# Kernel tuning notes

Hardware: AMD Instinct MI355X
Metric: run time of the kernel (lower is better)

The kernel has to match this reference:

```python
import jax, jax.numpy as jnp
import numpy as np

B = 8192
FL = 96      # feature_len
K = 3        # dynamic filter kernel size
NOUT = 2
EPS = 1e-5
P = (K - 1) // 2

def _lrelu(x):
    return jnp.where(x >= 0, x, 0.1 * x)

def _conv1d(x, w, b):
    # x: [b,1,L], w: [1,1,3], b: [1]; padding=1, stride=1
    y = jax.lax.conv_general_dilated(x, w, (1,), [(1, 1)], dimension_numbers=('NCH', 'OIH', 'NCH'))
    return y + b[None, :, None]

def _bn(y, g, be, m, v):
    # eval-mode BatchNorm1d with running stats
    return (y - m) / jnp.sqrt(v + EPS) * g + be


def setup_inputs() -> dict:
    key = jax.random.key(0)
    ks = jax.random.split(key, 40)
    d = {'x': jax.random.normal(ks[0], (B, 576), jnp.float32)}
    # trans_layer: 6 conv1d (1->1, k=3)
    for i in range(6):
        d[f'cw{i+1}'] = jax.random.normal(ks[1 + i], (1, 1, 3), jnp.float32) * 0.4
        d[f'cb{i+1}'] = jax.random.normal(ks[7 + i], (1,), jnp.float32) * 0.1
    # fusion_layer.de_dimen: Linear(FL -> K*K)
    d['de_W'] = jax.random.normal(ks[13], (K * K, FL), jnp.float32) * 0.1
    d['de_b'] = jnp.zeros((K * K,), jnp.float32)
    # reshape_layer: Linear(2*FL -> 3*FL) + BN
    d['rs_W'] = jax.random.normal(ks[14], (3 * FL, 2 * FL), jnp.float32) * 0.07
    d['rs_b'] = jnp.zeros((3 * FL,), jnp.float32)
    d['rs_g'] = 1.0 + 0.1 * jax.random.normal(ks[15], (3 * FL,), jnp.float32)
    d['rs_be'] = 0.1 * jax.random.normal(ks[16], (3 * FL,), jnp.float32)
    d['rs_m'] = 0.05 * jax.random.normal(ks[17], (3 * FL,), jnp.float32)
    d['rs_v'] = jax.random.uniform(ks[18], (3 * FL,), jnp.float32, 0.5, 1.5)
    # classifier_shallow: Linear(6*FL -> 3*FL) + BN + ReLU + Linear(3*FL -> NOUT)
    d['cl_W1'] = jax.random.normal(ks[19], (3 * FL, 6 * FL), jnp.float32) * 0.05
    d['cl_b1'] = jnp.zeros((3 * FL,), jnp.float32)
    d['cl_g'] = 1.0 + 0.1 * jax.random.normal(ks[20], (3 * FL,), jnp.float32)
    d['cl_be'] = 0.1 * jax.random.normal(ks[21], (3 * FL,), jnp.float32)
    d['cl_m'] = 0.05 * jax.random.normal(ks[22], (3 * FL,), jnp.float32)
    d['cl_v'] = jax.random.uniform(ks[23], (3 * FL,), jnp.float32, 0.5, 1.5)
    d['cl_W2'] = jax.random.normal(ks[24], (NOUT, 3 * FL), jnp.float32) * 0.05
    d['cl_b2'] = jnp.zeros((NOUT,), jnp.float32)
    return d


def reference(x, cw1, cb1, cw2, cb2, cw3, cb3, cw4, cb4, cw5, cb5, cw6, cb6,
              de_W, de_b, rs_W, rs_b, rs_g, rs_be, rs_m, rs_v,
              cl_W1, cl_b1, cl_g, cl_be, cl_m, cl_v, cl_W2, cl_b2):
    def trans(c):  # c: [b,1,3*FL] -> three [b,1,FL]
        s1, s2, s3 = c[..., :FL], c[..., FL:2 * FL], c[..., 2 * FL:]
        x1 = _lrelu(_conv1d(s1, cw1, cb1))
        x2 = _lrelu(_conv1d(s2, cw2, cb2))
        x3 = _lrelu(_conv1d(s3, cw3, cb3))
        return (_lrelu(_conv1d(x1, cw4, cb4)),
                _lrelu(_conv1d(x2, cw5, cb5)),
                _lrelu(_conv1d(x3, cw6, cb6)))

    def fusion(arm, x86, bert):  # each [b,1,FL]
        b = arm.shape[0]
        # c==1 so matmul(s_1^T, s_2) is a per-sample outer product: [b,FL,FL]
        m = _lrelu(jnp.einsum('bl,bm->blm', arm[:, 0], x86[:, 0]))
        # per-sample 3x3 dynamic filter from bert embedding
        s3 = _lrelu(bert[:, 0] @ de_W.T + de_b).reshape(b, 1, K, K)
        fe = jax.lax.conv_general_dilated(
            m.reshape(1, b, FL, FL), s3, (1, 1), [(P, P), (P, P)],
            feature_group_count=b, dimension_numbers=('NCHW', 'OIHW', 'NCHW'))
        fe = _lrelu(fe).reshape(b, FL, FL)
        # AvgPool1d(FL) == mean over last dim (and over rows for the permuted map)
        return jnp.concatenate([fe.mean(axis=2), fe.mean(axis=1)], axis=1)  # [b,2*FL]

    def resh(e):
        return _lrelu(_bn(e @ rs_W.T + rs_b, rs_g, rs_be, rs_m, rs_v))

    xu = x[:, None, :]  # unsqueeze(dim=1)
    c1, c2 = xu[..., :3 * FL], xu[..., 3 * FL:]
    e1 = resh(fusion(*trans(c1))) + c1[:, 0]
    e2 = resh(fusion(*trans(c2))) + c2[:, 0]
    ce = jnp.concatenate([e1, e2], axis=1)  # [b,6*FL]
    # Dropout is identity in eval mode
    h = jax.nn.relu(_bn(ce @ cl_W1.T + cl_b1, cl_g, cl_be, cl_m, cl_v))
    return h @ cl_W2.T + cl_b2  # [b,NOUT]
```

## Files before the change

kernel.cpp:

```cpp
#include <hip/hip_runtime.h>
#include <hip/hip_bf16.h>
#include <math.h>

#define FLn 96
#define SEG 288
#define EPRE_DIM 192
#define EPS_BN 1e-5f

typedef __attribute__((ext_vector_type(8))) short short8;
typedef __attribute__((ext_vector_type(4))) float floatx4;

__device__ __forceinline__ float lrelu(float v) { return fmaxf(v, 0.1f * v); }
__device__ __forceinline__ short f2bf(float f) {
  __hip_bfloat16 h = __float2bfloat16(f);
  return *reinterpret_cast<short*>(&h);
}

__global__ __launch_bounds__(256) void k0_cast(
    const float* __restrict__ rsW, const float* __restrict__ clW1,
    __hip_bfloat16* __restrict__ wB2, __hip_bfloat16* __restrict__ wB3) {
  int idx = blockIdx.x * 256 + threadIdx.x;
  int stride = gridDim.x * 256;
  for (int i = idx; i < 288 * 192; i += stride) wB2[i] = __float2bfloat16(rsW[i]);
  for (int i = idx; i < 288 * 576; i += stride) wB3[i] = __float2bfloat16(clW1[i]);
}

#define O_CIN 0
#define O_ST1 288
#define O_APP 576
#define O_ANP 674
#define O_XPP 772
#define O_XNP 870
#define O_BERT 968
#define O_WKER 1064
#define O_ABF 1088
#define O_BBF 1472
#define O_RP 0
#define SLICE 2048

__global__ __launch_bounds__(256) void k1_persample(
    const float* __restrict__ x,
    const float* __restrict__ cw1, const float* __restrict__ cb1,
    const float* __restrict__ cw2, const float* __restrict__ cb2,
    const float* __restrict__ cw3, const float* __restrict__ cb3,
    const float* __restrict__ cw4, const float* __restrict__ cb4,
    const float* __restrict__ cw5, const float* __restrict__ cb5,
    const float* __restrict__ cw6, const float* __restrict__ cb6,
    const float* __restrict__ deW, const float* __restrict__ deb,
    __hip_bfloat16* __restrict__ epre) {
  __shared__ float sl[4 * SLICE];
  const int tid = threadIdx.x;
  const int wave = tid >> 6;
  const int lane = tid & 63;
  const int quad = lane >> 4;
  const int l16 = lane & 15;
  const int unit = blockIdx.x * 4 + wave;
  float* S = sl + wave * SLICE;
  short* Ssh = (short*)S;
  const float* xrow = x + (size_t)(unit >> 1) * 576 + (unit & 1) * 288;

  const float a0w0 = cw1[0], a0w1 = cw1[1], a0w2 = cw1[2], a0b = cb1[0];
  const float a1w0 = cw2[0], a1w1 = cw2[1], a1w2 = cw2[2], a1b = cb2[0];
  const float a2w0 = cw3[0], a2w1 = cw3[1], a2w2 = cw3[2], a2b = cb3[0];
  const float b0w0 = cw4[0], b0w1 = cw4[1], b0w2 = cw4[2], b0b = cb4[0];
  const float b1w0 = cw5[0], b1w1 = cw5[1], b1w2 = cw5[2], b1b = cb5[0];
  const float b2w0 = cw6[0], b2w1 = cw6[1], b2w2 = cw6[2], b2b = cb6[0];

  for (int t4 = lane; t4 < 72; t4 += 64)
    *(float4*)&S[O_CIN + 4 * t4] = ((const float4*)xrow)[t4];
  if (lane < 8) S[576 + 98 * (lane >> 1) + (lane & 1) * 97] = 0.f;

  for (int t = lane; t < SEG; t += 64) {
    bool g1 = t >= 96, g2 = t >= 192;
    float wa = g2 ? a2w0 : (g1 ? a1w0 : a0w0);
    float wb = g2 ? a2w1 : (g1 ? a1w1 : a0w1);
    float wc = g2 ? a2w2 : (g1 ? a1w2 : a0w2);
    float bb = g2 ? a2b  : (g1 ? a1b  : a0b);
    int p = t - (g2 ? 192 : (g1 ? 96 : 0));
    float l = p > 0 ? S[O_CIN + t - 1] : 0.f;
    float m = S[O_CIN + t];
    float r = p < FLn - 1 ? S[O_CIN + t + 1] : 0.f;
    S[O_ST1 + t] = lrelu(fmaf(wa, l, fmaf(wb, m, fmaf(wc, r, bb))));
  }
  for (int t = lane; t < SEG; t += 64) {
    bool g1 = t >= 96, g2 = t >= 192;
    float wa = g2 ? b2w0 : (g1 ? b1w0 : b0w0);
    float wb = g2 ? b2w1 : (g1 ? b1w1 : b0w1);
    float wc = g2 ? b2w2 : (g1 ? b1w2 : b0w2);
    float bb = g2 ? b2b  : (g1 ? b1b  : b0b);
    int p = t - (g2 ? 192 : (g1 ? 96 : 0));
    float l = p > 0 ? S[O_ST1 + t - 1] : 0.f;
    float m = S[O_ST1 + t];
    float r = p < FLn - 1 ? S[O_ST1 + t + 1] : 0.f;
    float v = lrelu(fmaf(wa, l, fmaf(wb, m, fmaf(wc, r, bb))));
    if (!g1) {
      S[O_APP + 1 + p] = fmaxf(v, 0.1f * v);
      S[O_ANP + 1 + p] = fminf(v, 0.1f * v);
    } else if (!g2) {
      S[O_XPP + 1 + p] = fmaxf(v, 0.f);
      S[O_XNP + 1 + p] = fminf(v, 0.f);
    } else {
      S[O_BERT + p] = v;
    }
  }
  if (quad < 3) {
    float bv[6];
#pragma unroll
    for (int k = 0; k < 6; ++k) bv[k] = S[O_BERT + l16 + 16 * k];
#pragma unroll
    for (int oi = 0; oi < 3; ++oi) {
      int o = quad * 3 + oi;
      float p = 0.f;
#pragma unroll
      for (int k = 0; k < 6; ++k) p = fmaf(bv[k], deW[o * 96 + l16 + 16 * k], p);
      p += __shfl_xor(p, 1, 16);
      p += __shfl_xor(p, 2, 16);
      p += __shfl_xor(p, 4, 16);
      p += __shfl_xor(p, 8, 16);
      if (l16 == 0) S[O_WKER + o] = lrelu(p + deb[o]);
    }
  }
  float w9[9];
#pragma unroll
  for (int q = 0; q < 9; ++q) w9[q] = S[O_WKER + q];

  for (int t = lane; t < 96; t += 64) {
    float xp0 = S[O_XPP + t], xp1 = S[O_XPP + t + 1], xp2 = S[O_XPP + t + 2];
    float xn0 = S[O_XNP + t], xn1 = S[O_XNP + t + 1], xn2 = S[O_XNP + t + 2];
    short8 b;
#pragma unroll
    for (int d = 0; d < 3; ++d) {
      float cp = fmaf(w9[3 * d], xp0, fmaf(w9[3 * d + 1], xp1, w9[3 * d + 2] * xp2));
      float cn = fmaf(w9[3 * d], xn0, fmaf(w9[3 * d + 1], xn1, w9[3 * d + 2] * xn2));
      b[d] = f2bf(cp);
      b[3 + d] = f2bf(cn);
    }
    b[6] = 0; b[7] = 0;
    *(short8*)&Ssh[2 * O_BBF + t * 8] = b;
  }
  for (int m = lane; m < 96; m += 64) {
    short8 a;
    a[0] = f2bf(S[O_APP + m]);
    a[1] = f2bf(S[O_APP + m + 1]);
    a[2] = f2bf(S[O_APP + m + 2]);
    a[3] = f2bf(S[O_ANP + m]);
    a[4] = f2bf(S[O_ANP + m + 1]);
    a[5] = f2bf(S[O_ANP + m + 2]);
    a[6] = 0; a[7] = 0;
    *(short8*)&Ssh[2 * O_ABF + m * 8] = a;
  }

  short8 aF[6];
#pragma unroll
  for (int mt = 0; mt < 6; ++mt) {
    short8 t = *(const short8*)&Ssh[2 * O_ABF + (mt * 16 + l16) * 8];
#pragma unroll
    for (int j = 0; j < 8; ++j) aF[mt][j] = (quad == 0) ? t[j] : (short)0;
  }

  float rowpart[6][4];
#pragma unroll
  for (int mt = 0; mt < 6; ++mt)
#pragma unroll
    for (int r = 0; r < 4; ++r) rowpart[mt][r] = 0.f;
  float cs[6];
#pragma unroll
  for (int s = 0; s < 6; ++s) cs[s] = 0.f;

#pragma unroll
  for (int s = 0; s < 6; ++s) {
    short8 tb = *(const short8*)&Ssh[2 * O_BBF + (s * 16 + l16) * 8];
    short8 bF;
#pragma unroll
    for (int j = 0; j < 8; ++j) bF[j] = (quad == 0) ? tb[j] : (short)0;
    floatx4 accv[6];
#pragma unroll
    for (int mt = 0; mt < 6; ++mt)
      accv[mt] = __builtin_amdgcn_mfma_f32_16x16x32_bf16(
          aF[mt], bF, (floatx4){0.f, 0.f, 0.f, 0.f}, 0, 0, 0);
#pragma unroll
    for (int mt = 0; mt < 6; ++mt) {
#pragma unroll
      for (int r = 0; r < 4; ++r) {
        float sv = accv[mt][r];
        float f = fmaxf(sv, 0.1f * sv);
        rowpart[mt][r] += f;
        cs[s] += f;
      }
    }
  }

#pragma unroll
  for (int mt = 0; mt < 6; ++mt)
    *(float4*)&S[O_RP + (quad * 6 + mt) * 68 + l16 * 4] =
        make_float4(rowpart[mt][0], rowpart[mt][1], rowpart[mt][2], rowpart[mt][3]);
  for (int i = lane; i < 96; i += 64) {
    int g = ((i >> 2) & 3) * 6 + (i >> 4);
    int r = i & 3;
    float s = 0.f;
#pragma unroll
    for (int l = 0; l < 16; ++l) s += S[O_RP + g * 68 + l * 4 + r];
    epre[(size_t)unit * EPRE_DIM + i] = __float2bfloat16(s * (1.f / FLn));
  }
#pragma unroll
  for (int s = 0; s < 6; ++s) {
    float v = cs[s];
    v += __shfl_xor(v, 16, 64);
    v += __shfl_xor(v, 32, 64);
    if (quad == 0)
      epre[(size_t)unit * EPRE_DIM + FLn + s * 16 + l16] =
          __float2bfloat16(v * (1.f / FLn));
  }
}

__global__ __launch_bounds__(512) void k6_fused_tail(
    const short* __restrict__ epre, const short* __restrict__ wB2,
    const short* __restrict__ wB3, const float* __restrict__ x,
    const float* __restrict__ rsb, const float* __restrict__ rsg,
    const float* __restrict__ rsbe, const float* __restrict__ rsm,
    const float* __restrict__ rsv,
    const float* __restrict__ clb1, const float* __restrict__ clg,
    const float* __restrict__ clbe, const float* __restrict__ clm,
    const float* __restrict__ clv,
    const float* __restrict__ clW2, const float* __restrict__ clb2,
    float* __restrict__ out) {
  __shared__ short ceT[16 * 584];
  __shared__ float scr[8 * 32];
  const int tid = threadIdx.x;
  const int w = tid >> 6;
  const int lane = tid & 63;
  const int quad = lane >> 4;
  const int l16 = lane & 15;
  const int u0 = blockIdx.x * 32;
  const int s0 = blockIdx.x * 16;

  const int mt = w & 1;
  const int ng = w >> 1;
  short8 aF[6];
  {
    const short* arow = epre + (size_t)(u0 + mt * 16 + l16) * 192 + quad * 8;
#pragma unroll
    for (int kf = 0; kf < 6; ++kf) aF[kf] = *(const short8*)(arow + kf * 32);
  }

  for (int nf = ng; nf < 18; nf += 4) {
    const int n0 = nf * 16;
    const short* brow = wB2 + (size_t)(n0 + l16) * 192 + quad * 8;
    floatx4 acc = (floatx4){0.f, 0.f, 0.f, 0.f};
#pragma unroll
    for (int kf = 0; kf < 6; ++kf) {
      short8 bF = *(const short8*)(brow + kf * 32);
      acc = __builtin_amdgcn_mfma_f32_16x16x32_bf16(aF[kf], bF, acc, 0, 0, 0);
    }
    const int n = n0 + l16;
    const float sc = rsg[n] * rsqrtf(rsv[n] + EPS_BN);
    const float vb = rsb[n], mu = rsm[n], vbe = rsbe[n];
#pragma unroll
    for (int r = 0; r < 4; ++r) {
      int um = mt * 16 + quad * 4 + r;
      int trow = um >> 1;
      int cc = (um & 1) * 288 + n;
      float y = acc[r] + vb;
      float o = (y - mu) * sc + vbe;
      float e = lrelu(o) + x[(size_t)(s0 + trow) * 576 + cc];
      ceT[trow * 584 + cc] = f2bf(e);
    }
  }
  __syncthreads();

  float p0[4], p1[4];
#pragma unroll
  for (int r = 0; r < 4; ++r) { p0[r] = 0.f; p1[r] = 0.f; }

  for (int nt = w; nt < 18; nt += 8) {
    const int n0 = nt * 16;
    const short* brow = wB3 + (size_t)(n0 + l16) * 576 + quad * 8;
    floatx4 acc = (floatx4){0.f, 0.f, 0.f, 0.f};
#pragma unroll
    for (int kf = 0; kf < 18; ++kf) {
      short8 cF = *(const short8*)&ceT[l16 * 584 + kf * 32 + quad * 8];
      short8 bF = *(const short8*)(brow + kf * 32);
      acc = __builtin_amdgcn_mfma_f32_16x16x32_bf16(cF, bF, acc, 0, 0, 0);
    }
    const int n = n0 + l16;
    const float sc = clg[n] * rsqrtf(clv[n] + EPS_BN);
    const float vb = clb1[n], mu = clm[n], vbe = clbe[n];
    const float w2a = clW2[n], w2b = clW2[288 + n];
#pragma unroll
    for (int r = 0; r < 4; ++r) {
      float y = acc[r] + vb;
      float hh = fmaxf((y - mu) * sc + vbe, 0.f);
      p0[r] = fmaf(hh, w2a, p0[r]);
      p1[r] = fmaf(hh, w2b, p1[r]);
    }
  }
#pragma unroll
  for (int r = 0; r < 4; ++r) {
#pragma unroll
    for (int off = 1; off < 16; off <<= 1) {
      p0[r] += __shfl_xor(p0[r], off, 64);
      p1[r] += __shfl_xor(p1[r], off, 64);
    }
  }
  if (l16 == 0) {
#pragma unroll
    for (int r = 0; r < 4; ++r) {
      scr[w * 32 + (quad * 4 + r) * 2 + 0] = p0[r];
      scr[w * 32 + (quad * 4 + r) * 2 + 1] = p1[r];
    }
  }
  __syncthreads();
  if (tid < 32) {
    int row = tid >> 1, o = tid & 1;
    float s = 0.f;
#pragma unroll
    for (int g = 0; g < 8; ++g) s += scr[g * 32 + row * 2 + o];
    out[(size_t)(s0 + row) * 2 + o] = s + clb2[o];
  }
}

extern "C" void kernel_launch(void* const* d_in, const int* in_sizes, int n_in,
                              void* d_out, int out_size, void* d_ws, size_t ws_size,
                              hipStream_t stream) {
  const float* x   = (const float*)d_in[0];
  const float* cw1 = (const float*)d_in[1];  const float* cb1 = (const float*)d_in[2];
  const float* cw2 = (const float*)d_in[3];  const float* cb2 = (const float*)d_in[4];
  const float* cw3 = (const float*)d_in[5];  const float* cb3 = (const float*)d_in[6];
  const float* cw4 = (const float*)d_in[7];  const float* cb4 = (const float*)d_in[8];
  const float* cw5 = (const float*)d_in[9];  const float* cb5 = (const float*)d_in[10];
  const float* cw6 = (const float*)d_in[11]; const float* cb6 = (const float*)d_in[12];
  const float* deW = (const float*)d_in[13]; const float* deb = (const float*)d_in[14];
  const float* rsW = (const float*)d_in[15]; const float* rsb = (const float*)d_in[16];
  const float* rsg = (const float*)d_in[17]; const float* rsbe = (const float*)d_in[18];
  const float* rsm = (const float*)d_in[19]; const float* rsv = (const float*)d_in[20];
  const float* clW1 = (const float*)d_in[21]; const float* clb1 = (const float*)d_in[22];
  const float* clg = (const float*)d_in[23]; const float* clbe = (const float*)d_in[24];
  const float* clm = (const float*)d_in[25]; const float* clv = (const float*)d_in[26];
  const float* clW2 = (const float*)d_in[27]; const float* clb2 = (const float*)d_in[28];

  short* ws   = (short*)d_ws;
  short* epre = ws;
  short* wB2  = ws + 16384 * 192;
  short* wB3  = wB2 + 288 * 192;

  hipLaunchKernelGGL(k0_cast, dim3(128), dim3(256), 0, stream,
                     rsW, clW1, (__hip_bfloat16*)wB2, (__hip_bfloat16*)wB3);
  hipLaunchKernelGGL(k1_persample, dim3(4096), dim3(256), 0, stream, x,
                     cw1, cb1, cw2, cb2, cw3, cb3, cw4, cb4, cw5, cb5, cw6, cb6,
                     deW, deb, (__hip_bfloat16*)epre);
  hipLaunchKernelGGL(k6_fused_tail, dim3(512), dim3(512), 0, stream,
                     epre, wB2, wB3, x,
                     rsb, rsg, rsbe, rsm, rsv,
                     clb1, clg, clbe, clm, clv,
                     clW2, clb2, (float*)d_out);
}
```

Baseline: 217.0 us.

## Pre-swizzle weights and epre into MFMA fragment order for coalesced loads

The weight-cast kernel now writes rsW and clW1 in bf16, already arranged in the per-lane MFMA 16x16x32 fragment order. The per-sample kernel writes its pooled features in the same fragment-blocked layout. The tail kernel can then load each fragment as one contiguous 16-byte read per lane, with consecutive lanes adjacent, instead of strided row reads. The cost is more complex index math in the writers and scattered 2-byte stores in k0 and k1.

```diff
diff --git a/kernel.cpp b/kernel.cpp
--- a/kernel.cpp
+++ b/kernel.cpp
@@ -16,13 +16,25 @@
   return *reinterpret_cast<short*>(&h);
 }
 
-__global__ __launch_bounds__(256) void k0_cast(
+__global__ __launch_bounds__(256) void k0_swz(
     const float* __restrict__ rsW, const float* __restrict__ clW1,
-    __hip_bfloat16* __restrict__ wB2, __hip_bfloat16* __restrict__ wB3) {
+    short* __restrict__ wB2s, short* __restrict__ wB3s) {
   int idx = blockIdx.x * 256 + threadIdx.x;
   int stride = gridDim.x * 256;
-  for (int i = idx; i < 288 * 192; i += stride) wB2[i] = __float2bfloat16(rsW[i]);
-  for (int i = idx; i < 288 * 576; i += stride) wB3[i] = __float2bfloat16(clW1[i]);
+  for (int d = idx; d < 18 * 6 * 512; d += stride) {
+    int j = d & 7, lane = (d >> 3) & 63, t = d >> 9;
+    int kf = t % 6, nf = t / 6;
+    int n = nf * 16 + (lane & 15);
+    int k = kf * 32 + (lane >> 4) * 8 + j;
+    wB2s[d] = f2bf(rsW[n * 192 + k]);
+  }
+  for (int d = idx; d < 18 * 18 * 512; d += stride) {
+    int j = d & 7, lane = (d >> 3) & 63, t = d >> 9;
+    int kf = t % 18, nt = t / 18;
+    int n = nt * 16 + (lane & 15);
+    int k = kf * 32 + (lane >> 4) * 8 + j;
+    wB3s[d] = f2bf(clW1[n * 576 + k]);
+  }
 }
 
 #define O_CIN 0
@@ -47,7 +59,7 @@
     const float* __restrict__ cw5, const float* __restrict__ cb5,
     const float* __restrict__ cw6, const float* __restrict__ cb6,
     const float* __restrict__ deW, const float* __restrict__ deb,
-    __hip_bfloat16* __restrict__ epre) {
+    short* __restrict__ epre_s) {
   __shared__ float sl[4 * SLICE];
   const int tid = threadIdx.x;
   const int wave = tid >> 6;
@@ -194,28 +206,35 @@
   for (int mt = 0; mt < 6; ++mt)
     *(float4*)&S[O_RP + (quad * 6 + mt) * 68 + l16 * 4] =
         make_float4(rowpart[mt][0], rowpart[mt][1], rowpart[mt][2], rowpart[mt][3]);
+
+  const int g = unit >> 4;
+  const int u15 = unit & 15;
+  short* eb = epre_s + (size_t)g * 6 * 512;
   for (int i = lane; i < 96; i += 64) {
-    int g = ((i >> 2) & 3) * 6 + (i >> 4);
+    int gg = ((i >> 2) & 3) * 6 + (i >> 4);
     int r = i & 3;
     float s = 0.f;
 #pragma unroll
-    for (int l = 0; l < 16; ++l) s += S[O_RP + g * 68 + l * 4 + r];
-    epre[(size_t)unit * EPRE_DIM + i] = __float2bfloat16(s * (1.f / FLn));
+    for (int l = 0; l < 16; ++l) s += S[O_RP + gg * 68 + l * 4 + r];
+    int kf = i >> 5, rem = i & 31, q = rem >> 3, j = rem & 7;
+    eb[kf * 512 + (q * 16 + u15) * 8 + j] = f2bf(s * (1.f / FLn));
   }
 #pragma unroll
   for (int s = 0; s < 6; ++s) {
     float v = cs[s];
     v += __shfl_xor(v, 16, 64);
     v += __shfl_xor(v, 32, 64);
-    if (quad == 0)
-      epre[(size_t)unit * EPRE_DIM + FLn + s * 16 + l16] =
-          __float2bfloat16(v * (1.f / FLn));
+    if (quad == 0) {
+      int kidx = 96 + s * 16 + l16;
+      int kf = kidx >> 5, rem = kidx & 31, q = rem >> 3, j = rem & 7;
+      eb[kf * 512 + (q * 16 + u15) * 8 + j] = f2bf(v * (1.f / FLn));
+    }
   }
 }
 
 __global__ __launch_bounds__(512) void k6_fused_tail(
-    const short* __restrict__ epre, const short* __restrict__ wB2,
-    const short* __restrict__ wB3, const float* __restrict__ x,
+    const short* __restrict__ epre_s, const short* __restrict__ wB2s,
+    const short* __restrict__ wB3s, const float* __restrict__ x,
     const float* __restrict__ rsb, const float* __restrict__ rsg,
     const float* __restrict__ rsbe, const float* __restrict__ rsm,
     const float* __restrict__ rsv,
@@ -231,28 +250,26 @@
   const int lane = tid & 63;
   const int quad = lane >> 4;
   const int l16 = lane & 15;
-  const int u0 = blockIdx.x * 32;
   const int s0 = blockIdx.x * 16;
 
   const int mt = w & 1;
   const int ng = w >> 1;
   short8 aF[6];
   {
-    const short* arow = epre + (size_t)(u0 + mt * 16 + l16) * 192 + quad * 8;
-#pragma unroll
-    for (int kf = 0; kf < 6; ++kf) aF[kf] = *(const short8*)(arow + kf * 32);
+    const short* arow = epre_s + (size_t)(blockIdx.x * 2 + mt) * 6 * 512 + lane * 8;
+#pragma unroll
+    for (int kf = 0; kf < 6; ++kf) aF[kf] = *(const short8*)(arow + kf * 512);
   }
 
   for (int nf = ng; nf < 18; nf += 4) {
-    const int n0 = nf * 16;
-    const short* brow = wB2 + (size_t)(n0 + l16) * 192 + quad * 8;
+    const short* brow = wB2s + (size_t)nf * 6 * 512 + lane * 8;
     floatx4 acc = (floatx4){0.f, 0.f, 0.f, 0.f};
 #pragma unroll
     for (int kf = 0; kf < 6; ++kf) {
-      short8 bF = *(const short8*)(brow + kf * 32);
+      short8 bF = *(const short8*)(brow + kf * 512);
       acc = __builtin_amdgcn_mfma_f32_16x16x32_bf16(aF[kf], bF, acc, 0, 0, 0);
     }
-    const int n = n0 + l16;
+    const int n = nf * 16 + l16;
     const float sc = rsg[n] * rsqrtf(rsv[n] + EPS_BN);
     const float vb = rsb[n], mu = rsm[n], vbe = rsbe[n];
 #pragma unroll
@@ -273,16 +290,15 @@
   for (int r = 0; r < 4; ++r) { p0[r] = 0.f; p1[r] = 0.f; }
 
   for (int nt = w; nt < 18; nt += 8) {
-    const int n0 = nt * 16;
-    const short* brow = wB3 + (size_t)(n0 + l16) * 576 + quad * 8;
+    const short* brow = wB3s + (size_t)nt * 18 * 512 + lane * 8;
     floatx4 acc = (floatx4){0.f, 0.f, 0.f, 0.f};
 #pragma unroll
     for (int kf = 0; kf < 18; ++kf) {
       short8 cF = *(const short8*)&ceT[l16 * 584 + kf * 32 + quad * 8];
-      short8 bF = *(const short8*)(brow + kf * 32);
+      short8 bF = *(const short8*)(brow + kf * 512);
       acc = __builtin_amdgcn_mfma_f32_16x16x32_bf16(cF, bF, acc, 0, 0, 0);
     }
-    const int n = n0 + l16;
+    const int n = nt * 16 + l16;
     const float sc = clg[n] * rsqrtf(clv[n] + EPS_BN);
     const float vb = clb1[n], mu = clm[n], vbe = clbe[n];
     const float w2a = clW2[n], w2b = clW2[288 + n];
@@ -338,18 +354,18 @@
   const float* clm = (const float*)d_in[25]; const float* clv = (const float*)d_in[26];
   const float* clW2 = (const float*)d_in[27]; const float* clb2 = (const float*)d_in[28];
 
-  short* ws   = (short*)d_ws;
-  short* epre = ws;
-  short* wB2  = ws + 16384 * 192;
-  short* wB3  = wB2 + 288 * 192;
-
-  hipLaunchKernelGGL(k0_cast, dim3(128), dim3(256), 0, stream,
-                     rsW, clW1, (__hip_bfloat16*)wB2, (__hip_bfloat16*)wB3);
+  short* ws    = (short*)d_ws;
+  short* epre_s = ws;
+  short* wB2s  = ws + 16384 * 192;
+  short* wB3s  = wB2s + 18 * 6 * 512;
+
+  hipLaunchKernelGGL(k0_swz, dim3(128), dim3(256), 0, stream,
+                     rsW, clW1, wB2s, wB3s);
   hipLaunchKernelGGL(k1_persample, dim3(4096), dim3(256), 0, stream, x,
                      cw1, cb1, cw2, cb2, cw3, cb3, cw4, cb4, cw5, cb5, cw6, cb6,
-                     deW, deb, (__hip_bfloat16*)epre);
+                     deW, deb, epre_s);
   hipLaunchKernelGGL(k6_fused_tail, dim3(512), dim3(512), 0, stream,
-                     epre, wB2, wB3, x,
+                     epre_s, wB2s, wB3s, x,
                      rsb, rsg, rsbe, rsm, rsv,
                      clb1, clg, clbe, clm, clv,
                      clW2, clb2, (float*)d_out);
```

Result: faster. 201.5 us (-7.2%).
